# Kernel tuning notes

Hardware: AMD Instinct MI355X
Metric: run time of the kernel (lower is better)

## Reference

```python
import jax, jax.numpy as jnp
import numpy as np

ALPHA = 0.7
EPS = 1e-12


def setup_inputs() -> dict:
    key = jax.random.key(0)
    k1, k2, k3, k4 = jax.random.split(key, 4)
    B, P, D = 4, 256, 384  # dinov2_vits14: 224/14=16 -> 256 patches, dim 384
    N, M = 100000, 2000    # local memory bank (max_memory), global bank (train images)
    return {
        "patches": jax.random.normal(k1, (B, P, D), dtype=jnp.float32),
        "globals_x": jax.random.normal(k2, (B, D), dtype=jnp.float32),
        "mb_local": jax.random.normal(k3, (N, D), dtype=jnp.float32),
        "mb_global": jax.random.normal(k4, (M, D), dtype=jnp.float32),
    }


def _l2_normalize(x):
    return x / (jnp.linalg.norm(x, axis=-1, keepdims=True) + EPS)


def reference(patches, globals_x, mb_local, mb_global):
    # Token normalization as in _extract_patch_tokens / _extract_global
    p = _l2_normalize(patches)    # [B, P, D]
    g = _l2_normalize(globals_x)  # [B, D]

    # Local: Euclidean cdist(p_i, MB_local) via gram trick, min over bank, max over patches
    p_sq = jnp.sum(p * p, axis=-1)                      # [B, P]
    mbl_sq = jnp.sum(mb_local * mb_local, axis=-1)      # [N]
    d2 = (p_sq[..., None] + mbl_sq[None, None, :]
          - 2.0 * jnp.einsum('bpd,nd->bpn', p, mb_local))  # [B, P, N]
    d = jnp.sqrt(jnp.maximum(d2, 0.0))
    local_score = jnp.max(jnp.min(d, axis=2), axis=1)   # [B]

    # Global: cdist(g_i, MB_global).min()
    g_sq = jnp.sum(g * g, axis=-1)                      # [B]
    mbg_sq = jnp.sum(mb_global * mb_global, axis=-1)    # [M]
    gd2 = g_sq[:, None] + mbg_sq[None, :] - 2.0 * (g @ mb_global.T)  # [B, M]
    gdist = jnp.min(jnp.sqrt(jnp.maximum(gd2, 0.0)), axis=1)         # [B]

    return ALPHA * local_score + (1.0 - ALPHA) * gdist  # [B] anomaly scores
```

## Files before the change

kernel.cpp:

```cpp
#include <hip/hip_runtime.h>
#include <math.h>


#define D 384
#define PQ 256
#define TNP 128
#define BK 64
#define NCH 6
#define LROW 72

typedef __attribute__((ext_vector_type(8))) short short8v;
typedef __attribute__((ext_vector_type(4))) float f32x4;

static __device__ __forceinline__ unsigned short f2bf(float f) {
  unsigned u = __float_as_uint(f);
  unsigned r = 0x7FFFu + ((u >> 16) & 1u);
  return (unsigned short)((u + r) >> 16);
}
static __device__ __forceinline__ unsigned pack2(float lo, float hi) {
  return (unsigned)f2bf(lo) | ((unsigned)f2bf(hi) << 16);
}

__global__ void prep_kernel(const float* __restrict__ patches,
                            const float* __restrict__ globals_x,
                            float* __restrict__ pf32,
                            unsigned short* __restrict__ pbf,
                            float* __restrict__ psq,
                            float* __restrict__ gf32,
                            float* __restrict__ gsq,
                            int Q) {
  const int row = blockIdx.x;
  const int lane = threadIdx.x;
  const float* src = (row < Q) ? (patches + (size_t)row * D)
                               : (globals_x + (size_t)(row - Q) * D);
  float v[6];
  float ss = 0.f;
#pragma unroll
  for (int j = 0; j < 6; ++j) { v[j] = src[lane + 64 * j]; ss += v[j] * v[j]; }
#pragma unroll
  for (int d = 1; d < 64; d <<= 1) ss += __shfl_xor(ss, d);
  const float inv = 1.f / (sqrtf(ss) + 1e-12f);
  float pn[6]; float ps = 0.f;
#pragma unroll
  for (int j = 0; j < 6; ++j) { pn[j] = v[j] * inv; ps += pn[j] * pn[j]; }
#pragma unroll
  for (int d = 1; d < 64; d <<= 1) ps += __shfl_xor(ps, d);
  if (row < Q) {
#pragma unroll
    for (int j = 0; j < 6; ++j) {
      pf32[(size_t)row * D + lane + 64 * j] = pn[j];
      pbf[(size_t)row * D + lane + 64 * j] = f2bf(pn[j]);
    }
    if (lane == 0) psq[row] = ps;
  } else {
    const int b = row - Q;
#pragma unroll
    for (int j = 0; j < 6; ++j) gf32[(size_t)b * D + lane + 64 * j] = pn[j];
    if (lane == 0) gsq[b] = ps;
  }
}

__device__ __forceinline__ void atomic_fmin(float* addr, float val) {
  unsigned* ua = (unsigned*)addr;
  float cur = __uint_as_float(atomicAdd(ua, 0u));
  while (val < cur) {
    unsigned assumed = __float_as_uint(cur);
    unsigned old = atomicCAS(ua, assumed, __float_as_uint(val));
    if (old == assumed) break;
    cur = __uint_as_float(old);
  }
}

template <int MODE>
__global__ __launch_bounds__(256, 2) void score_kernel(
    const float* __restrict__ mbl,
    const unsigned short* __restrict__ pbf,
    float* __restrict__ tilemin,
    int Q, int N) {
  __shared__ alignas(16) unsigned short lB0[TNP * LROW];
  __shared__ alignas(16) unsigned short lB1[TNP * LROW];
  __shared__ float msqH[TNP * 2];
  __shared__ float msqF[TNP];

  const int tid = threadIdx.x;
  const int lane = tid & 63;
  const int wid = tid >> 6;
  const int wq = wid >> 1;
  const int wn = wid & 1;
  const int qp = blockIdx.x;
  const int nb = blockIdx.y;
  const int qbase = qp * PQ;
  const int nbase = nb * TNP;
  const int fr = lane & 15;
  const int g = lane >> 4;

  const int brow = tid >> 1, h = tid & 1;
  const int gn = nbase + brow;
  const bool nvalid = gn < N;
  const float* bptr = mbl + (size_t)(nvalid ? gn : 0) * D + h * 32;
  const int boff = brow * LROW + h * 32;

  const unsigned short* abase = pbf + (size_t)(qbase + wq * 128 + fr) * D + g * 8;

  f32x4 acc[8][4];
#pragma unroll
  for (int i = 0; i < 8; ++i)
#pragma unroll
    for (int j = 0; j < 4; ++j) acc[i][j] = (f32x4){0.f, 0.f, 0.f, 0.f};
  float msqreg = 0.f;

  auto stage = [&](int kc, unsigned short* dst) {
    const float* src = bptr + kc * BK;
    uint4 w[4];
    if (nvalid) {
      float s = 0.f;
#pragma unroll
      for (int i = 0; i < 4; ++i) {
        float4 f0 = *(const float4*)(src + i * 8);
        float4 f1 = *(const float4*)(src + i * 8 + 4);
        s += f0.x*f0.x + f0.y*f0.y + f0.z*f0.z + f0.w*f0.w
           + f1.x*f1.x + f1.y*f1.y + f1.z*f1.z + f1.w*f1.w;
        w[i] = (uint4){ pack2(f0.x,f0.y), pack2(f0.z,f0.w), pack2(f1.x,f1.y), pack2(f1.z,f1.w) };
      }
      msqreg += s;
    } else {
#pragma unroll
      for (int i = 0; i < 4; ++i) w[i] = (uint4){0u,0u,0u,0u};
    }
#pragma unroll
    for (int i = 0; i < 4; ++i) *(uint4*)(dst + boff + i * 8) = w[i];
  };

  auto compute = [&](int kc, const unsigned short* buf) {
#pragma unroll
    for (int ks = 0; ks < 2; ++ks) {
      short8v b[4];
#pragma unroll
      for (int nf = 0; nf < 4; ++nf)
        b[nf] = *(const short8v*)(&buf[(wn * 64 + nf * 16 + fr) * LROW + (ks * 4 + g) * 8]);
#pragma unroll
      for (int mf = 0; mf < 8; ++mf) {
        short8v av = *(const short8v*)(abase + (size_t)mf * 16 * D + kc * BK + ks * 32);
#pragma unroll
        for (int nf = 0; nf < 4; ++nf)
          acc[mf][nf] = __builtin_amdgcn_mfma_f32_16x16x32_bf16(av, b[nf], acc[mf][nf], 0, 0, 0);
      }
    }
  };

  stage(0, lB0);
  __syncthreads();
  stage(1, lB1);
  compute(0, lB0);
  __syncthreads();
  stage(2, lB0);
  compute(1, lB1);
  __syncthreads();
  stage(3, lB1);
  compute(2, lB0);
  __syncthreads();
  stage(4, lB0);
  compute(3, lB1);
  __syncthreads();
  stage(5, lB1);
  compute(4, lB0);
  __syncthreads();
  compute(5, lB1);
  __syncthreads();

  msqH[tid] = msqreg;
  __syncthreads();
  if (tid < TNP) msqF[tid] = (nbase + tid < N) ? (msqH[2 * tid] + msqH[2 * tid + 1]) : 1e30f;
  __syncthreads();

  float mq[4];
#pragma unroll
  for (int nf = 0; nf < 4; ++nf) mq[nf] = msqF[wn * 64 + nf * 16 + fr];

#pragma unroll
  for (int mf = 0; mf < 8; ++mf) {
#pragma unroll
    for (int j = 0; j < 4; ++j) {
      float v0 = fminf(mq[0] - 2.f * acc[mf][0][j], mq[1] - 2.f * acc[mf][1][j]);
      float v1 = fminf(mq[2] - 2.f * acc[mf][2][j], mq[3] - 2.f * acc[mf][3][j]);
#pragma unroll
      for (int d2 = 1; d2 < 16; d2 <<= 1) {
        v0 = fminf(v0, __shfl_xor(v0, d2));
        v1 = fminf(v1, __shfl_xor(v1, d2));
      }
      if (fr == 0) {
        const int q = qbase + wq * 128 + mf * 16 + g * 4 + j;
        if (MODE == 0) {
          tilemin[(size_t)(nb * 4 + wn * 2 + 0) * Q + q] = v0;
          tilemin[(size_t)(nb * 4 + wn * 2 + 1) * Q + q] = v1;
        } else {
          atomic_fmin(&tilemin[q], fminf(v0, v1));
        }
      }
    }
  }
}

__global__ void init_inf_kernel(float* __restrict__ p, int n) {
  int i = blockIdx.x * 256 + threadIdx.x;
  if (i < n) p[i] = 1e30f;
}
__global__ void final_dmin_kernel(const float* __restrict__ d2min,
                                  const float* __restrict__ psq,
                                  float* __restrict__ dmin, int Q) {
  int q = blockIdx.x * 256 + threadIdx.x;
  if (q < Q) dmin[q] = sqrtf(fmaxf(psq[q] + d2min[q], 0.f));
}

__global__ __launch_bounds__(256) void transpose_kernel(
    const float* __restrict__ tm, float* __restrict__ tmT, int Q, int NSUBP) {
  __shared__ float t[64][65];
  const int tx = threadIdx.x & 63, ty = threadIdx.x >> 6;
  const int qb = blockIdx.x * 64, sb = blockIdx.y * 64;
#pragma unroll
  for (int i = 0; i < 64; i += 4)
    t[i + ty][tx] = tm[(size_t)(sb + i + ty) * Q + qb + tx];
  __syncthreads();
#pragma unroll
  for (int i = 0; i < 64; i += 4)
    tmT[(size_t)(qb + i + ty) * NSUBP + sb + tx] = t[tx][i + ty];
}

__device__ __forceinline__ float block_min(float v, float* red) {
#pragma unroll
  for (int d = 1; d < 64; d <<= 1) v = fminf(v, __shfl_xor(v, d));
  if ((threadIdx.x & 63) == 0) red[threadIdx.x >> 6] = v;
  __syncthreads();
  const float r = fminf(fminf(red[0], red[1]), fminf(red[2], red[3]));
  __syncthreads();
  return r;
}
__device__ __forceinline__ float block_max(float v, float* red) {
#pragma unroll
  for (int d = 1; d < 64; d <<= 1) v = fmaxf(v, __shfl_xor(v, d));
  if ((threadIdx.x & 63) == 0) red[threadIdx.x >> 6] = v;
  __syncthreads();
  const float r = fmaxf(fmaxf(red[0], red[1]), fmaxf(red[2], red[3]));
  __syncthreads();
  return r;
}

__global__ __launch_bounds__(256) void refine_kernel(
    const float* __restrict__ mbl,
    const float* __restrict__ pf32,
    const float* __restrict__ psq,
    const float* __restrict__ tmT,
    float* __restrict__ dmin,
    int Q, int N, int NSUB, int NSUBP) {
  __shared__ int cnt;
  __shared__ int cand[64];
  __shared__ float red[4];
  const int q = blockIdx.x;
  const int tid = threadIdx.x;
  if (tid == 0) cnt = 0;
  __syncthreads();

  const float* rowp = tmT + (size_t)q * NSUBP;
  float m = 1e30f;
  for (int r = tid; r < NSUB; r += 256) m = fminf(m, rowp[r]);
  const float gm = block_min(m, red);
  const float thr = gm + 0.25f;

  for (int r = tid; r < NSUB; r += 256)
    if (rowp[r] <= thr) { int i = atomicAdd(&cnt, 1); if (i < 64) cand[i] = r; }
  __syncthreads();
  const int nc = min(cnt, 64);

  const int row8 = tid >> 3, oct = tid & 7;
  const float* prow = pf32 + (size_t)q * D + oct * 48;
  float4 pr[12];
#pragma unroll
  for (int i = 0; i < 12; ++i) pr[i] = *(const float4*)(prow + i * 4);

  float best = 1e30f;
  for (int c = 0; c < nc; ++c) {
    const int n = cand[c] * 32 + row8;
    float v;
    if (n < N) {
      const float* mr = mbl + (size_t)n * D + oct * 48;
      float dot = 0.f, ms = 0.f;
#pragma unroll
      for (int i = 0; i < 12; ++i) {
        float4 a = *(const float4*)(mr + i * 4);
        dot += a.x*pr[i].x + a.y*pr[i].y + a.z*pr[i].z + a.w*pr[i].w;
        ms  += a.x*a.x + a.y*a.y + a.z*a.z + a.w*a.w;
      }
      v = ms - 2.f * dot;
    } else {
      v = 1e30f;
    }
#pragma unroll
    for (int d2 = 1; d2 < 8; d2 <<= 1) {
      float o = __shfl_xor(v, d2);
      v = (n < N) ? v + o : 1e30f;
    }
    best = fminf(best, v);
  }
  best = block_min(best, red);
  if (tid == 0) dmin[q] = sqrtf(fmaxf(psq[q] + best, 0.f));
}

__global__ __launch_bounds__(256) void gmin_kernel(
    const float* __restrict__ mbg,
    const float* __restrict__ gf32,
    const float* __restrict__ gsq,
    float* __restrict__ gpartG,
    int M) {
  __shared__ float red[4];
  const int b = blockIdx.x, s = blockIdx.y;
  const int tid = threadIdx.x;
  const int sl = (M + 31) / 32;
  const int row = s * sl + tid;
  const float* g = gf32 + (size_t)b * D;
  float v = 1e30f;
  if (tid < sl && row < M) {
    const float* mr = mbg + (size_t)row * D;
    float dot = 0.f, ms = 0.f;
#pragma unroll 4
    for (int k = 0; k < D; k += 4) {
      float4 a = *(const float4*)(mr + k);
      float4 p = *(const float4*)(g + k);
      dot += a.x*p.x + a.y*p.y + a.z*p.z + a.w*p.w;
      ms  += a.x*a.x + a.y*a.y + a.z*a.z + a.w*a.w;
    }
    v = gsq[b] + ms - 2.f * dot;
  }
  v = block_min(v, red);
  if (tid == 0) gpartG[b * 32 + s] = v;
}

__global__ __launch_bounds__(256) void out_kernel(
    const float* __restrict__ gpartG,
    const float* __restrict__ dmin,
    float* __restrict__ out,
    int P) {
  __shared__ float red[4];
  const int b = blockIdx.x;
  const int tid = threadIdx.x;
  float v = (tid < P) ? dmin[(size_t)b * P + tid] : -1e30f;
  const float local = block_max(v, red);
  float gm = (tid < 32) ? gpartG[b * 32 + tid] : 1e30f;
  gm = block_min(gm, red);
  if (tid == 0) out[b] = 0.7f * local + 0.3f * sqrtf(fmaxf(gm, 0.f));
}

extern "C" void kernel_launch(void* const* d_in, const int* in_sizes, int n_in,
                              void* d_out, int out_size, void* d_ws, size_t ws_size,
                              hipStream_t stream) {
  const float* patches   = (const float*)d_in[0];
  const float* globals_x = (const float*)d_in[1];
  const float* mbl       = (const float*)d_in[2];
  const float* mbg       = (const float*)d_in[3];
  float* out = (float*)d_out;

  const int Q = in_sizes[0] / D;
  const int B = in_sizes[1] / D;
  const int N = in_sizes[2] / D;
  const int M = in_sizes[3] / D;
  const int P = Q / B;
  const int NPAN = (N + TNP - 1) / TNP;
  const int NSUB = NPAN * 4;
  const int NSUBP = ((NSUB + 63) / 64) * 64;
  const int QP = (Q + PQ - 1) / PQ;

  char* w = (char*)d_ws;
  char* wend = (char*)d_ws + ws_size;
  auto alloc = [&](size_t bytes) {
    char* p = w;
    w += (bytes + 255) & ~(size_t)255;
    return p;
  };
  float*          pf32   = (float*)alloc((size_t)Q * D * sizeof(float));
  unsigned short* pbf    = (unsigned short*)alloc((size_t)Q * D * sizeof(unsigned short));
  float*          psq    = (float*)alloc((size_t)Q * sizeof(float));
  float*          gf32   = (float*)alloc((size_t)B * D * sizeof(float));
  float*          gsqp   = (float*)alloc((size_t)B * sizeof(float));
  float*          dmin   = (float*)alloc((size_t)Q * sizeof(float));
  float*          gpartG = (float*)alloc((size_t)B * 32 * sizeof(float));
  float*          d2min  = (float*)alloc((size_t)Q * sizeof(float));
  if (w > wend) return;

  const size_t tm_bytes = (size_t)NSUBP * Q * sizeof(float);
  const int full = (w + 2 * ((tm_bytes + 255) & ~(size_t)255) <= wend) ? 1 : 0;

  prep_kernel<<<Q + B, 64, 0, stream>>>(patches, globals_x, pf32, pbf, psq, gf32, gsqp, Q);

  if (full) {
    float* tilemin  = (float*)alloc(tm_bytes);
    float* tileminT = (float*)alloc(tm_bytes);
    score_kernel<0><<<dim3(QP, NPAN), 256, 0, stream>>>(mbl, pbf, tilemin, Q, N);
    transpose_kernel<<<dim3(Q / 64, NSUBP / 64), 256, 0, stream>>>(tilemin, tileminT, Q, NSUBP);
    refine_kernel<<<Q, 256, 0, stream>>>(mbl, pf32, psq, tileminT, dmin, Q, N, NSUB, NSUBP);
  } else {
    init_inf_kernel<<<(Q + 255) / 256, 256, 0, stream>>>(d2min, Q);
    score_kernel<1><<<dim3(QP, NPAN), 256, 0, stream>>>(mbl, pbf, d2min, Q, N);
    final_dmin_kernel<<<(Q + 255) / 256, 256, 0, stream>>>(d2min, psq, dmin, Q);
  }

  gmin_kernel<<<dim3(B, 32), 256, 0, stream>>>(mbg, gf32, gsqp, gpartG, M);
  out_kernel<<<B, 256, 0, stream>>>(gpartG, dmin, out, P);
}
```

Before: 517.6 us.

## Remap score waves to full-N tiles, prefetch A/B in registers, XCD-aware block order

Each wave now covers 64 query rows across all 128 bank rows instead of a 128x64 quadrant, so A fragments are loaded once per k-chunk and B is read from LDS for all 8 n-fragments. Global loads for the next B chunk and the A fragments are issued into registers before the MFMA compute, with the bf16 conversion and LDS write after it, to overlap memory latency with compute. Workgroups are launched as a flat grid and remapped so that consecutive tiles sharing the same bank panel land on the same XCD for L2 reuse. Register pressure rises from the prefetch buffers and the wider B fragment set, which may reduce occupancy.

New measurement: 491.7 us. -5.0%, faster.

```diff
diff --git a/kernel.cpp b/kernel.cpp
--- a/kernel.cpp
+++ b/kernel.cpp
@@ -6,7 +6,6 @@
 #define PQ 256
 #define TNP 128
 #define BK 64
-#define NCH 6
 #define LROW 72
 
 typedef __attribute__((ext_vector_type(8))) short short8v;
@@ -76,7 +75,7 @@
     const float* __restrict__ mbl,
     const unsigned short* __restrict__ pbf,
     float* __restrict__ tilemin,
-    int Q, int N) {
+    int Q, int N, int QP, int q8, int r8) {
   __shared__ alignas(16) unsigned short lB0[TNP * LROW];
   __shared__ alignas(16) unsigned short lB1[TNP * LROW];
   __shared__ float msqH[TNP * 2];
@@ -85,116 +84,116 @@
   const int tid = threadIdx.x;
   const int lane = tid & 63;
   const int wid = tid >> 6;
-  const int wq = wid >> 1;
-  const int wn = wid & 1;
-  const int qp = blockIdx.x;
-  const int nb = blockIdx.y;
+  const int fr = lane & 15;
+  const int g = lane >> 4;
+
+  const int flat = blockIdx.x;
+  const int xcd = flat & 7, idx = flat >> 3;
+  const int wg = (xcd < r8 ? xcd * (q8 + 1) : r8 * (q8 + 1) + (xcd - r8) * q8) + idx;
+  const int nb = wg / QP;
+  const int qp = wg - nb * QP;
   const int qbase = qp * PQ;
   const int nbase = nb * TNP;
-  const int fr = lane & 15;
-  const int g = lane >> 4;
 
   const int brow = tid >> 1, h = tid & 1;
   const int gn = nbase + brow;
-  const bool nvalid = gn < N;
-  const float* bptr = mbl + (size_t)(nvalid ? gn : 0) * D + h * 32;
+  const float* bptr = mbl + (size_t)((gn < N) ? gn : 0) * D + h * 32;
   const int boff = brow * LROW + h * 32;
 
-  const unsigned short* abase = pbf + (size_t)(qbase + wq * 128 + fr) * D + g * 8;
-
-  f32x4 acc[8][4];
-#pragma unroll
-  for (int i = 0; i < 8; ++i)
-#pragma unroll
-    for (int j = 0; j < 4; ++j) acc[i][j] = (f32x4){0.f, 0.f, 0.f, 0.f};
+  const unsigned short* abase = pbf + (size_t)(qbase + wid * 64 + fr) * D + g * 8;
+
+  f32x4 acc[4][8];
+#pragma unroll
+  for (int i = 0; i < 4; ++i)
+#pragma unroll
+    for (int j = 0; j < 8; ++j) acc[i][j] = (f32x4){0.f, 0.f, 0.f, 0.f};
   float msqreg = 0.f;
-
-  auto stage = [&](int kc, unsigned short* dst) {
+  float4 breg[8];
+  short8v a[8];
+
+  auto bload = [&](int kc) {
     const float* src = bptr + kc * BK;
+#pragma unroll
+    for (int i = 0; i < 8; ++i) breg[i] = *(const float4*)(src + i * 4);
+  };
+  auto bwrite = [&](unsigned short* base) {
+    float s = 0.f;
     uint4 w[4];
-    if (nvalid) {
-      float s = 0.f;
-#pragma unroll
-      for (int i = 0; i < 4; ++i) {
-        float4 f0 = *(const float4*)(src + i * 8);
-        float4 f1 = *(const float4*)(src + i * 8 + 4);
-        s += f0.x*f0.x + f0.y*f0.y + f0.z*f0.z + f0.w*f0.w
-           + f1.x*f1.x + f1.y*f1.y + f1.z*f1.z + f1.w*f1.w;
-        w[i] = (uint4){ pack2(f0.x,f0.y), pack2(f0.z,f0.w), pack2(f1.x,f1.y), pack2(f1.z,f1.w) };
-      }
-      msqreg += s;
-    } else {
-#pragma unroll
-      for (int i = 0; i < 4; ++i) w[i] = (uint4){0u,0u,0u,0u};
-    }
-#pragma unroll
-    for (int i = 0; i < 4; ++i) *(uint4*)(dst + boff + i * 8) = w[i];
+#pragma unroll
+    for (int i = 0; i < 4; ++i) {
+      float4 f0 = breg[2 * i], f1 = breg[2 * i + 1];
+      s += f0.x*f0.x + f0.y*f0.y + f0.z*f0.z + f0.w*f0.w
+         + f1.x*f1.x + f1.y*f1.y + f1.z*f1.z + f1.w*f1.w;
+      w[i] = (uint4){ pack2(f0.x,f0.y), pack2(f0.z,f0.w), pack2(f1.x,f1.y), pack2(f1.z,f1.w) };
+    }
+#pragma unroll
+    for (int i = 0; i < 4; ++i) *(uint4*)(base + boff + i * 8) = w[i];
+    msqreg += s;
   };
-
-  auto compute = [&](int kc, const unsigned short* buf) {
+  auto aload = [&](int kc) {
+#pragma unroll
+    for (int ks = 0; ks < 2; ++ks)
+#pragma unroll
+      for (int mf = 0; mf < 4; ++mf)
+        a[ks * 4 + mf] = *(const short8v*)(abase + (size_t)mf * 16 * D + kc * BK + ks * 32);
+  };
+  auto compute = [&](const unsigned short* buf) {
 #pragma unroll
     for (int ks = 0; ks < 2; ++ks) {
-      short8v b[4];
-#pragma unroll
-      for (int nf = 0; nf < 4; ++nf)
-        b[nf] = *(const short8v*)(&buf[(wn * 64 + nf * 16 + fr) * LROW + (ks * 4 + g) * 8]);
-#pragma unroll
-      for (int mf = 0; mf < 8; ++mf) {
-        short8v av = *(const short8v*)(abase + (size_t)mf * 16 * D + kc * BK + ks * 32);
-#pragma unroll
-        for (int nf = 0; nf < 4; ++nf)
-          acc[mf][nf] = __builtin_amdgcn_mfma_f32_16x16x32_bf16(av, b[nf], acc[mf][nf], 0, 0, 0);
-      }
+      short8v b[8];
+#pragma unroll
+      for (int nf = 0; nf < 8; ++nf)
+        b[nf] = *(const short8v*)(&buf[(nf * 16 + fr) * LROW + (ks * 4 + g) * 8]);
+#pragma unroll
+      for (int mf = 0; mf < 4; ++mf)
+#pragma unroll
+        for (int nf = 0; nf < 8; ++nf)
+          acc[mf][nf] = __builtin_amdgcn_mfma_f32_16x16x32_bf16(a[ks * 4 + mf], b[nf],
+                                                                acc[mf][nf], 0, 0, 0);
     }
   };
 
-  stage(0, lB0);
-  __syncthreads();
-  stage(1, lB1);
-  compute(0, lB0);
-  __syncthreads();
-  stage(2, lB0);
-  compute(1, lB1);
-  __syncthreads();
-  stage(3, lB1);
-  compute(2, lB0);
-  __syncthreads();
-  stage(4, lB0);
-  compute(3, lB1);
-  __syncthreads();
-  stage(5, lB1);
-  compute(4, lB0);
-  __syncthreads();
-  compute(5, lB1);
-  __syncthreads();
+  bload(0);
+  bwrite(lB0);
+  __syncthreads();
+  aload(0); bload(1); compute(lB0); bwrite(lB1); __syncthreads();
+  aload(1); bload(2); compute(lB1); bwrite(lB0); __syncthreads();
+  aload(2); bload(3); compute(lB0); bwrite(lB1); __syncthreads();
+  aload(3); bload(4); compute(lB1); bwrite(lB0); __syncthreads();
+  aload(4); bload(5); compute(lB0); bwrite(lB1); __syncthreads();
+  aload(5);           compute(lB1);              __syncthreads();
 
   msqH[tid] = msqreg;
   __syncthreads();
   if (tid < TNP) msqF[tid] = (nbase + tid < N) ? (msqH[2 * tid] + msqH[2 * tid + 1]) : 1e30f;
   __syncthreads();
 
-  float mq[4];
-#pragma unroll
-  for (int nf = 0; nf < 4; ++nf) mq[nf] = msqF[wn * 64 + nf * 16 + fr];
-
-#pragma unroll
-  for (int mf = 0; mf < 8; ++mf) {
+  float mq[8];
+#pragma unroll
+  for (int nf = 0; nf < 8; ++nf) mq[nf] = msqF[nf * 16 + fr];
+
+#pragma unroll
+  for (int mf = 0; mf < 4; ++mf) {
 #pragma unroll
     for (int j = 0; j < 4; ++j) {
-      float v0 = fminf(mq[0] - 2.f * acc[mf][0][j], mq[1] - 2.f * acc[mf][1][j]);
-      float v1 = fminf(mq[2] - 2.f * acc[mf][2][j], mq[3] - 2.f * acc[mf][3][j]);
-#pragma unroll
-      for (int d2 = 1; d2 < 16; d2 <<= 1) {
-        v0 = fminf(v0, __shfl_xor(v0, d2));
-        v1 = fminf(v1, __shfl_xor(v1, d2));
-      }
+      float v[4];
+#pragma unroll
+      for (int s = 0; s < 4; ++s)
+        v[s] = fminf(mq[2 * s] - 2.f * acc[mf][2 * s][j],
+                     mq[2 * s + 1] - 2.f * acc[mf][2 * s + 1][j]);
+#pragma unroll
+      for (int d2 = 1; d2 < 16; d2 <<= 1)
+#pragma unroll
+        for (int s = 0; s < 4; ++s) v[s] = fminf(v[s], __shfl_xor(v[s], d2));
       if (fr == 0) {
-        const int q = qbase + wq * 128 + mf * 16 + g * 4 + j;
+        const int q = qbase + wid * 64 + mf * 16 + g * 4 + j;
         if (MODE == 0) {
-          tilemin[(size_t)(nb * 4 + wn * 2 + 0) * Q + q] = v0;
-          tilemin[(size_t)(nb * 4 + wn * 2 + 1) * Q + q] = v1;
+#pragma unroll
+          for (int s = 0; s < 4; ++s)
+            tilemin[(size_t)(nb * 4 + s) * Q + q] = v[s];
         } else {
-          atomic_fmin(&tilemin[q], fminf(v0, v1));
+          atomic_fmin(&tilemin[q],
+                      fminf(fminf(v[0], v[1]), fminf(v[2], v[3])));
         }
       }
     }
@@ -286,9 +285,9 @@
       float dot = 0.f, ms = 0.f;
 #pragma unroll
       for (int i = 0; i < 12; ++i) {
-        float4 a = *(const float4*)(mr + i * 4);
-        dot += a.x*pr[i].x + a.y*pr[i].y + a.z*pr[i].z + a.w*pr[i].w;
-        ms  += a.x*a.x + a.y*a.y + a.z*a.z + a.w*a.w;
+        float4 aa = *(const float4*)(mr + i * 4);
+        dot += aa.x*pr[i].x + aa.y*pr[i].y + aa.z*pr[i].z + aa.w*pr[i].w;
+        ms  += aa.x*aa.x + aa.y*aa.y + aa.z*aa.z + aa.w*aa.w;
       }
       v = ms - 2.f * dot;
     } else {
@@ -323,10 +322,10 @@
     float dot = 0.f, ms = 0.f;
 #pragma unroll 4
     for (int k = 0; k < D; k += 4) {
-      float4 a = *(const float4*)(mr + k);
+      float4 aa = *(const float4*)(mr + k);
       float4 p = *(const float4*)(g + k);
-      dot += a.x*p.x + a.y*p.y + a.z*p.z + a.w*p.w;
-      ms  += a.x*a.x + a.y*a.y + a.z*a.z + a.w*a.w;
+      dot += aa.x*p.x + aa.y*p.y + aa.z*p.z + aa.w*p.w;
+      ms  += aa.x*aa.x + aa.y*aa.y + aa.z*aa.z + aa.w*aa.w;
     }
     v = gsq[b] + ms - 2.f * dot;
   }
@@ -367,6 +366,8 @@
   const int NSUB = NPAN * 4;
   const int NSUBP = ((NSUB + 63) / 64) * 64;
   const int QP = (Q + PQ - 1) / PQ;
+  const int nwg = QP * NPAN;
+  const int q8 = nwg / 8, r8 = nwg % 8;
 
   char* w = (char*)d_ws;
   char* wend = (char*)d_ws + ws_size;
@@ -393,12 +394,12 @@
   if (full) {
     float* tilemin  = (float*)alloc(tm_bytes);
     float* tileminT = (float*)alloc(tm_bytes);
-    score_kernel<0><<<dim3(QP, NPAN), 256, 0, stream>>>(mbl, pbf, tilemin, Q, N);
+    score_kernel<0><<<nwg, 256, 0, stream>>>(mbl, pbf, tilemin, Q, N, QP, q8, r8);
     transpose_kernel<<<dim3(Q / 64, NSUBP / 64), 256, 0, stream>>>(tilemin, tileminT, Q, NSUBP);
     refine_kernel<<<Q, 256, 0, stream>>>(mbl, pf32, psq, tileminT, dmin, Q, N, NSUB, NSUBP);
   } else {
     init_inf_kernel<<<(Q + 255) / 256, 256, 0, stream>>>(d2min, Q);
-    score_kernel<1><<<dim3(QP, NPAN), 256, 0, stream>>>(mbl, pbf, d2min, Q, N);
+    score_kernel<1><<<nwg, 256, 0, stream>>>(mbl, pbf, d2min, Q, N, QP, q8, r8);
     final_dmin_kernel<<<(Q + 255) / 256, 256, 0, stream>>>(d2min, psq, dmin, Q);
   }
 
```
